# Kernel tuning notes

Measured on AMD Instinct MI355X. Metric: run time of the kernel, lower is better.

The kernel has to match this reference:

```python
import jax, jax.numpy as jnp
import numpy as np

D_MODEL = 1024
NUM_HEAD = 16
D_K = D_MODEL // NUM_HEAD


def setup_inputs() -> dict:
    key = jax.random.key(0)
    ks = jax.random.split(key, 11)
    B, S = 2, 2048
    s = 1.0 / np.sqrt(D_MODEL)
    return {
        "q": jax.random.normal(ks[0], (B, S, D_MODEL), jnp.float32),
        "k": jax.random.normal(ks[1], (B, S, D_MODEL), jnp.float32),
        "v": jax.random.normal(ks[2], (B, S, D_MODEL), jnp.float32),
        "Wq": jax.random.normal(ks[3], (D_MODEL, D_MODEL), jnp.float32) * s,
        "bq": jnp.zeros((D_MODEL,), jnp.float32),
        "Wk": jax.random.normal(ks[4], (D_MODEL, D_MODEL), jnp.float32) * s,
        "bk": jnp.zeros((D_MODEL,), jnp.float32),
        "Wv": jax.random.normal(ks[5], (D_MODEL, D_MODEL), jnp.float32) * s,
        "bv": jnp.zeros((D_MODEL,), jnp.float32),
        "Wo": jax.random.normal(ks[6], (D_MODEL, D_MODEL), jnp.float32) * s,
        "bo": jnp.zeros((D_MODEL,), jnp.float32),
    }


def _split_head(x, B):
    # [B, S, d_model] -> [B, H, S, d_k]
    S = x.shape[1]
    return x.reshape(B, S, NUM_HEAD, D_K).transpose(0, 2, 1, 3)


def reference(q, k, v, Wq, bq, Wk, bk, Wv, bv, Wo, bo):
    B = q.shape[0]
    qh = _split_head(q @ Wq + bq, B)  # [B,H,Sq,dk]
    kh = _split_head(k @ Wk + bk, B)  # [B,H,Sk,dk]
    vh = _split_head(v @ Wv + bv, B)  # [B,H,Sk,dk]
    scores = jnp.einsum("bhqd,bhkd->bhqk", qh, kh) / jnp.sqrt(
        jnp.asarray(D_K, qh.dtype)
    )
    attn = jax.nn.softmax(scores, axis=-1)
    out = jnp.einsum("bhqk,bhkd->bhqd", attn, vh)  # [B,H,Sq,dk]
    out = out.transpose(0, 2, 1, 3).reshape(B, -1, D_MODEL)
    return jax.nn.relu(out @ Wo + bo)
```

## Files before the change

### kernel.cpp

```cpp
#include <hip/hip_runtime.h>
#include <math.h>

#define SEQ 2048
#define NHD 16

typedef float f32x4 __attribute__((ext_vector_type(4), may_alias));
typedef _Float16 h16x8 __attribute__((ext_vector_type(8), may_alias));
typedef _Float16 h16x4 __attribute__((ext_vector_type(4), may_alias));

__device__ __forceinline__ void gl_lds16(const void* g, void* l) {
  __builtin_amdgcn_global_load_lds(
      (const __attribute__((address_space(1))) unsigned int*)g,
      (__attribute__((address_space(3))) unsigned int*)l, 16, 0, 0);
}

struct PrepArgs {
  const float* W[4];
  _Float16* T[4];
  const float* X[3];
  _Float16* H[3];
};

__global__ __launch_bounds__(256) void prep_k(PrepArgs a) {
  __shared__ float tile[64][65];
  const int blk = blockIdx.x;
  const int t = threadIdx.x;
  if (blk < 1024) {
    const int widx = blk >> 8, tl = blk & 255;
    const int nb = (tl & 15) * 64, kb = (tl >> 4) * 64;
    const float* __restrict__ W = a.W[widx];
    _Float16* __restrict__ T = a.T[widx];
    const int c = t & 63, r0 = t >> 6;
#pragma unroll
    for (int i = 0; i < 16; ++i) {
      const int r = i * 4 + r0;
      tile[r][c] = W[(size_t)(kb + r) * 1024 + nb + c];
    }
    __syncthreads();
#pragma unroll
    for (int i = 0; i < 16; ++i) {
      const int n = i * 4 + r0;
      T[(size_t)(nb + n) * 1024 + kb + c] = (_Float16)tile[c][n];
    }
  } else {
    const int b2 = blk - 1024;
    const int z = b2 >> 11, bx = b2 & 2047;
    const float* __restrict__ X = a.X[z];
    _Float16* __restrict__ H = a.H[z];
    const size_t i = ((size_t)bx * 256 + t) * 8;
    const f32x4 f0 = *(const f32x4*)(X + i);
    const f32x4 f1 = *(const f32x4*)(X + i + 4);
    const float fs[8] = {f0.x, f0.y, f0.z, f0.w, f1.x, f1.y, f1.z, f1.w};
    h16x8 o;
#pragma unroll
    for (int j = 0; j < 8; ++j) o[j] = (_Float16)fs[j];
    *(h16x8*)(H + i) = o;
  }
}

__global__ __launch_bounds__(256) void vtrans_k(const unsigned short* __restrict__ Vb,
                                                unsigned short* __restrict__ Vt) {
  __shared__ unsigned short tile[64][65];
  const int t = threadIdx.x;
  const int c = t & 63, r0 = t >> 6;
  const int s0 = blockIdx.x * 64;
  const int bh = blockIdx.y;
#pragma unroll
  for (int i = 0; i < 16; ++i) {
    const int r = i * 4 + r0;
    tile[r][c] = Vb[((size_t)bh * SEQ + s0 + r) * 64 + c];
  }
  __syncthreads();
#pragma unroll
  for (int i = 0; i < 16; ++i) {
    const int d = i * 4 + r0;
    const int sp = ((c & 15) * 4) + (c >> 4);
    Vt[((size_t)bh * 64 + d) * SEQ + s0 + sp] = tile[c][d];
  }
}

struct QKVArgs {
  const _Float16* A[3];
  const _Float16* Bt[3];
  const float* bias[3];
  _Float16* C[3];
};

__global__ __launch_bounds__(256, 4) void gemm_qkv_k(QKVArgs a) {
  __shared__ char smem[16384];
  h16x8* lds8 = (h16x8*)smem;
  const int dblk = blockIdx.x;
  const int z = dblk >> 8;
  const int rb = dblk & 255;
  const int n0 = ((rb >> 3) & 7) * 128;
  const int m0 = ((((rb >> 6) << 3) | (rb & 7))) * 128;
  const _Float16* __restrict__ A = a.A[z];
  const _Float16* __restrict__ Bt = a.Bt[z];
  const float* __restrict__ bias = a.bias[z];
  _Float16* __restrict__ C = a.C[z];

  const int t = threadIdx.x;
  const int l = t & 63, w = t >> 6;
  const int quad = l >> 4, l15 = l & 15;
  const int wm = w >> 1, wn = w & 1;

  const f32x4 z4 = {0.f, 0.f, 0.f, 0.f};
  f32x4 acc[4][4];
#pragma unroll
  for (int i = 0; i < 4; ++i)
#pragma unroll
    for (int j = 0; j < 4; ++j) acc[i][j] = z4;

  for (int k0 = 0; k0 < 1024; k0 += 32) {
#pragma unroll
    for (int it = 0; it < 2; ++it) {
      const int c = it * 4 + w;
      const int rr = c * 16 + l15;
      gl_lds16(A + (size_t)(m0 + rr) * 1024 + k0 + quad * 8, smem + c * 1024);
      gl_lds16(Bt + (size_t)(n0 + rr) * 1024 + k0 + quad * 8, smem + 8192 + c * 1024);
    }
    __syncthreads();
    h16x8 af[4], bf[4];
#pragma unroll
    for (int i = 0; i < 4; ++i) {
      af[i] = lds8[(wm * 4 + i) * 64 + l];
      bf[i] = lds8[512 + (wn * 4 + i) * 64 + l];
    }
#pragma unroll
    for (int i = 0; i < 4; ++i)
#pragma unroll
      for (int j = 0; j < 4; ++j)
        acc[i][j] = __builtin_amdgcn_mfma_f32_16x16x32_f16(af[i], bf[j], acc[i][j], 0, 0, 0);
    __syncthreads();
  }
#pragma unroll
  for (int i = 0; i < 4; ++i)
#pragma unroll
    for (int j = 0; j < 4; ++j) {
      const int col = n0 + wn * 64 + j * 16 + l15;
      const float bv = bias[col];
#pragma unroll
      for (int r = 0; r < 4; ++r) {
        const int row = m0 + wm * 64 + i * 16 + quad * 4 + r;
        const int b = row >> 11, s = row & 2047;
        const int h = col >> 6, d = col & 63;
        C[((size_t)(b * NHD + h) * SEQ + s) * 64 + d] = (_Float16)(acc[i][j][r] + bv);
      }
    }
}

__global__ __launch_bounds__(256, 4) void gemm_o_k(
    const _Float16* __restrict__ Op0, const _Float16* __restrict__ Op1,
    const float* __restrict__ Lp, const _Float16* __restrict__ Bt,
    const float* __restrict__ bias, float* __restrict__ Cf) {
  __shared__ char smem[24576];
  h16x8* lds8 = (h16x8*)smem;
  float* inv_lds = (float*)(smem + 16384);
  const int rb = blockIdx.x;
  const int n0 = ((rb >> 3) & 7) * 128;
  const int m0 = ((((rb >> 6) << 3) | (rb & 7))) * 128;
  const int t = threadIdx.x;
  const int l = t & 63, w = t >> 6;
  const int quad = l >> 4, l15 = l & 15;
  const int wm = w >> 1, wn = w & 1;

#pragma unroll
  for (int e = t; e < 2048; e += 256) {
    const int rl = e >> 4, hh = e & 15;
    const int m = m0 + rl;
    const int b = m >> 11, s = m & 2047;
    const size_t li = (size_t)(b * NHD + hh) * 2048 + s;
    inv_lds[e] = 1.f / (Lp[li] + Lp[65536 + li]);
  }
  __syncthreads();

  const f32x4 z4 = {0.f, 0.f, 0.f, 0.f};
  f32x4 acc[4][4];
#pragma unroll
  for (int i = 0; i < 4; ++i)
#pragma unroll
    for (int j = 0; j < 4; ++j) acc[i][j] = z4;

  for (int k0 = 0; k0 < 1024; k0 += 32) {
#pragma unroll
    for (int it = 0; it < 2; ++it) {
      const int c = it * 4 + w;
      const int rr = c * 16 + l15;
      gl_lds16(Bt + (size_t)(n0 + rr) * 1024 + k0 + quad * 8, smem + 8192 + c * 1024);
    }
    const int head = k0 >> 6;
#pragma unroll
    for (int it = 0; it < 2; ++it) {
      const int row = it * 64 + (t >> 2);
      const int aq = t & 3;
      const int slot = (row >> 4) * 64 + aq * 16 + ((row & 15) ^ (aq * 2));
      const size_t off = (size_t)(m0 + row) * 1024 + k0 + aq * 8;
      const h16x8 a0 = *(const h16x8*)(Op0 + off);
      const h16x8 a1 = *(const h16x8*)(Op1 + off);
      const float inv = inv_lds[row * 16 + head];
      h16x8 hv;
#pragma unroll
      for (int j = 0; j < 8; ++j)
        hv[j] = (_Float16)(((float)a0[j] + (float)a1[j]) * inv);
      lds8[slot] = hv;
    }
    __syncthreads();
    h16x8 af[4], bf[4];
#pragma unroll
    for (int i = 0; i < 4; ++i) {
      af[i] = lds8[(wm * 4 + i) * 64 + quad * 16 + (l15 ^ (quad * 2))];
      bf[i] = lds8[512 + (wn * 4 + i) * 64 + l];
    }
#pragma unroll
    for (int i = 0; i < 4; ++i)
#pragma unroll
      for (int j = 0; j < 4; ++j)
        acc[i][j] = __builtin_amdgcn_mfma_f32_16x16x32_f16(af[i], bf[j], acc[i][j], 0, 0, 0);
    __syncthreads();
  }
#pragma unroll
  for (int i = 0; i < 4; ++i)
#pragma unroll
    for (int j = 0; j < 4; ++j) {
      const int col = n0 + wn * 64 + j * 16 + l15;
      const float bv = bias[col];
#pragma unroll
      for (int r = 0; r < 4; ++r) {
        const int row = m0 + wm * 64 + i * 16 + quad * 4 + r;
        Cf[(size_t)row * 1024 + col] = fmaxf(acc[i][j][r] + bv, 0.f);
      }
    }
}

__global__ __launch_bounds__(256, 4) void attn_k(
    const _Float16* __restrict__ Qf, const _Float16* __restrict__ Kf,
    const _Float16* __restrict__ Vtp,
    _Float16* __restrict__ Op0, _Float16* __restrict__ Op1,
    float* __restrict__ Lp) {
  __shared__ char smem[34816];
  h16x8* lds8 = (h16x8*)smem;
  const int dblk = blockIdx.x;
  const int comb = ((dblk >> 7) << 3) | (dblk & 7);
  const int q0 = ((dblk >> 3) & 15) * 128;
  const int bh = comb >> 1;
  const int kz = comb & 1;
  const int t = threadIdx.x;
  const int l = t & 63, w = t >> 6;
  const int quad = l >> 4, l15 = l & 15;
  const int b = bh >> 4, h = bh & 15;

  const _Float16* Kb = Kf + (size_t)bh * SEQ * 64;
  const _Float16* Vtb = Vtp + (size_t)bh * 64 * SEQ;

  h16x8 qf[2][2];
#pragma unroll
  for (int mi = 0; mi < 2; ++mi) {
    const size_t qb = ((size_t)bh * SEQ + q0 + w * 32 + mi * 16 + l15) * 64;
#pragma unroll
    for (int ks = 0; ks < 2; ++ks)
      qf[mi][ks] = *(const h16x8*)&Qf[qb + ks * 32 + quad * 8];
  }
  const f32x4 z4 = {0.f, 0.f, 0.f, 0.f};
  f32x4 oacc[2][4], lacc[2];
#pragma unroll
  for (int mi = 0; mi < 2; ++mi) {
    lacc[mi] = z4;
#pragma unroll
    for (int i = 0; i < 4; ++i) oacc[mi][i] = z4;
  }
  h16x8 ones;
#pragma unroll
  for (int j = 0; j < 8; ++j) ones[j] = (_Float16)1.0f;

  const int kbeg = kz * 1024;
  for (int k0 = kbeg; k0 < kbeg + 1024; k0 += 64) {
#pragma unroll
    for (int it = 0; it < 2; ++it) {
      const int c = it * 4 + w;
      const int kd = (c >> 1) * 16 + l15;
      const int off2 = (c & 1) * 32 + quad * 8;
      gl_lds16(Kb + (size_t)(k0 + kd) * 64 + off2, smem + c * 1024);
      gl_lds16(Vtb + (size_t)kd * SEQ + k0 + off2, smem + 8192 + c * 1024);
    }
    __syncthreads();

    {
      h16x8 kfr[4][2];
#pragma unroll
      for (int nt = 0; nt < 4; ++nt)
#pragma unroll
        for (int ks = 0; ks < 2; ++ks) kfr[nt][ks] = lds8[(nt * 2 + ks) * 64 + l];

#pragma unroll
      for (int mi = 0; mi < 2; ++mi) {
        f32x4 sacc[4];
#pragma unroll
        for (int nt = 0; nt < 4; ++nt) {
          f32x4 s = z4;
          s = __builtin_amdgcn_mfma_f32_16x16x32_f16(qf[mi][0], kfr[nt][0], s, 0, 0, 0);
          s = __builtin_amdgcn_mfma_f32_16x16x32_f16(qf[mi][1], kfr[nt][1], s, 0, 0, 0);
          sacc[nt] = s;
        }
        char* pb = smem + 16384 + (w * 2 + mi) * 2304;
#pragma unroll
        for (int r = 0; r < 4; ++r) {
          h16x4 pk;
#pragma unroll
          for (int nt = 0; nt < 4; ++nt)
            pk[nt] = (_Float16)__expf(sacc[nt][r] * 0.125f);
          *(h16x4*)(pb + (quad * 4 + r) * 144 + l15 * 8) = pk;
        }
      }
    }
    __asm__ __volatile__("" ::: "memory");

    {
      h16x8 vfr[4][2];
#pragma unroll
      for (int nt = 0; nt < 4; ++nt)
#pragma unroll
        for (int ks = 0; ks < 2; ++ks) vfr[nt][ks] = lds8[512 + (nt * 2 + ks) * 64 + l];

#pragma unroll
      for (int mi = 0; mi < 2; ++mi) {
        char* pb = smem + 16384 + (w * 2 + mi) * 2304;
        const h16x8 pf0 = *(const h16x8*)(pb + l15 * 144 + quad * 16);
        const h16x8 pf1 = *(const h16x8*)(pb + l15 * 144 + 64 + quad * 16);
        lacc[mi] = __builtin_amdgcn_mfma_f32_16x16x32_f16(pf0, ones, lacc[mi], 0, 0, 0);
        lacc[mi] = __builtin_amdgcn_mfma_f32_16x16x32_f16(pf1, ones, lacc[mi], 0, 0, 0);
#pragma unroll
        for (int nt = 0; nt < 4; ++nt) {
          oacc[mi][nt] = __builtin_amdgcn_mfma_f32_16x16x32_f16(pf0, vfr[nt][0], oacc[mi][nt], 0, 0, 0);
          oacc[mi][nt] = __builtin_amdgcn_mfma_f32_16x16x32_f16(pf1, vfr[nt][1], oacc[mi][nt], 0, 0, 0);
        }
      }
    }
    __syncthreads();
  }

  _Float16* __restrict__ Op = kz ? Op1 : Op0;
#pragma unroll
  for (int mi = 0; mi < 2; ++mi)
#pragma unroll
    for (int nt = 0; nt < 4; ++nt)
#pragma unroll
      for (int r = 0; r < 4; ++r) {
        const size_t tok = (size_t)b * SEQ + q0 + w * 32 + mi * 16 + quad * 4 + r;
        Op[tok * 1024 + h * 64 + nt * 16 + l15] = (_Float16)oacc[mi][nt][r];
      }
  if (l15 == 0) {
#pragma unroll
    for (int mi = 0; mi < 2; ++mi)
#pragma unroll
      for (int r = 0; r < 4; ++r) {
        const int row = q0 + w * 32 + mi * 16 + quad * 4 + r;
        Lp[(size_t)kz * 65536 + bh * 2048 + row] = lacc[mi][r];
      }
  }
}

extern "C" void kernel_launch(void* const* d_in, const int* in_sizes, int n_in,
                              void* d_out, int out_size, void* d_ws, size_t ws_size,
                              hipStream_t stream) {
  const float* q = (const float*)d_in[0];
  const float* k = (const float*)d_in[1];
  const float* v = (const float*)d_in[2];
  const float* Wq = (const float*)d_in[3];
  const float* bq = (const float*)d_in[4];
  const float* Wk = (const float*)d_in[5];
  const float* bk = (const float*)d_in[6];
  const float* Wv = (const float*)d_in[7];
  const float* bv = (const float*)d_in[8];
  const float* Wo = (const float*)d_in[9];
  const float* bo = (const float*)d_in[10];

  char* W8 = (char*)d_ws;
  const size_t MB = 1024 * 1024;
  auto F = [&](size_t off) { return (_Float16*)(W8 + off); };
  _Float16* wt[4] = {F(0), F(2 * MB), F(4 * MB), F(6 * MB)};
  _Float16* qf = F(8 * MB);
  _Float16* kf = F(16 * MB);
  _Float16* vf = F(24 * MB);
  _Float16* Qf = F(32 * MB);
  _Float16* Kf = F(40 * MB);
  _Float16* Vb = F(48 * MB);
  _Float16* Vt = F(56 * MB);
  _Float16* Op0 = F(8 * MB);
  _Float16* Op1 = F(16 * MB);
  float* Lp = (float*)(W8 + 64 * MB);

  const dim3 blk(256);

  PrepArgs pa;
  pa.W[0] = Wq; pa.W[1] = Wk; pa.W[2] = Wv; pa.W[3] = Wo;
  pa.T[0] = wt[0]; pa.T[1] = wt[1]; pa.T[2] = wt[2]; pa.T[3] = wt[3];
  pa.X[0] = q; pa.X[1] = k; pa.X[2] = v;
  pa.H[0] = qf; pa.H[1] = kf; pa.H[2] = vf;
  prep_k<<<dim3(7168), blk, 0, stream>>>(pa);

  QKVArgs qa;
  qa.A[0] = qf; qa.A[1] = kf; qa.A[2] = vf;
  qa.Bt[0] = wt[0]; qa.Bt[1] = wt[1]; qa.Bt[2] = wt[2];
  qa.bias[0] = bq; qa.bias[1] = bk; qa.bias[2] = bv;
  qa.C[0] = Qf; qa.C[1] = Kf; qa.C[2] = Vb;
  gemm_qkv_k<<<dim3(768), blk, 0, stream>>>(qa);

  vtrans_k<<<dim3(32, 32), blk, 0, stream>>>((const unsigned short*)Vb,
                                             (unsigned short*)Vt);
  attn_k<<<dim3(1024), blk, 0, stream>>>(Qf, Kf, Vt, Op0, Op1, Lp);
  gemm_o_k<<<dim3(256), blk, 0, stream>>>(Op0, Op1, Lp, wt[3], bo, (float*)d_out);
}
```

Measured before the change: 254.8 us.

## Double-buffer LDS tiles in QKV and output projection GEMMs

Both projection GEMMs now use two LDS buffers. The next K-slice's global-to-LDS loads (and, in the output GEMM, the register prefetch of the attention partials) are issued before the MFMAs on the current slice, and one barrier per iteration replaces two. The aim is to hide global load latency behind matrix math. In exchange, LDS use doubles, which may reduce occupancy, and the output GEMM drops its min-blocks launch bound, which could raise register pressure.

```diff
diff --git a/kernel.cpp b/kernel.cpp
--- a/kernel.cpp
+++ b/kernel.cpp
@@ -87,8 +87,7 @@
 };
 
 __global__ __launch_bounds__(256, 4) void gemm_qkv_k(QKVArgs a) {
-  __shared__ char smem[16384];
-  h16x8* lds8 = (h16x8*)smem;
+  __shared__ char smem[32768];
   const int dblk = blockIdx.x;
   const int z = dblk >> 8;
   const int rb = dblk & 255;
@@ -104,22 +103,31 @@
   const int quad = l >> 4, l15 = l & 15;
   const int wm = w >> 1, wn = w & 1;
 
-  const f32x4 z4 = {0.f, 0.f, 0.f, 0.f};
-  f32x4 acc[4][4];
-#pragma unroll
-  for (int i = 0; i < 4; ++i)
-#pragma unroll
-    for (int j = 0; j < 4; ++j) acc[i][j] = z4;
-
-  for (int k0 = 0; k0 < 1024; k0 += 32) {
+  auto stage = [&](int buf, int k0) {
 #pragma unroll
     for (int it = 0; it < 2; ++it) {
       const int c = it * 4 + w;
       const int rr = c * 16 + l15;
-      gl_lds16(A + (size_t)(m0 + rr) * 1024 + k0 + quad * 8, smem + c * 1024);
-      gl_lds16(Bt + (size_t)(n0 + rr) * 1024 + k0 + quad * 8, smem + 8192 + c * 1024);
-    }
-    __syncthreads();
+      gl_lds16(A + (size_t)(m0 + rr) * 1024 + k0 + quad * 8,
+               smem + buf * 16384 + c * 1024);
+      gl_lds16(Bt + (size_t)(n0 + rr) * 1024 + k0 + quad * 8,
+               smem + buf * 16384 + 8192 + c * 1024);
+    }
+  };
+
+  const f32x4 z4 = {0.f, 0.f, 0.f, 0.f};
+  f32x4 acc[4][4];
+#pragma unroll
+  for (int i = 0; i < 4; ++i)
+#pragma unroll
+    for (int j = 0; j < 4; ++j) acc[i][j] = z4;
+
+  stage(0, 0);
+  __syncthreads();
+  int cur = 0;
+  for (int k0 = 0; k0 < 1024; k0 += 32) {
+    if (k0 + 32 < 1024) stage(cur ^ 1, k0 + 32);
+    const h16x8* lds8 = (const h16x8*)(smem + cur * 16384);
     h16x8 af[4], bf[4];
 #pragma unroll
     for (int i = 0; i < 4; ++i) {
@@ -132,6 +140,7 @@
       for (int j = 0; j < 4; ++j)
         acc[i][j] = __builtin_amdgcn_mfma_f32_16x16x32_f16(af[i], bf[j], acc[i][j], 0, 0, 0);
     __syncthreads();
+    cur ^= 1;
   }
 #pragma unroll
   for (int i = 0; i < 4; ++i)
@@ -149,13 +158,12 @@
     }
 }
 
-__global__ __launch_bounds__(256, 4) void gemm_o_k(
+__global__ __launch_bounds__(256) void gemm_o_k(
     const _Float16* __restrict__ Op0, const _Float16* __restrict__ Op1,
     const float* __restrict__ Lp, const _Float16* __restrict__ Bt,
     const float* __restrict__ bias, float* __restrict__ Cf) {
-  __shared__ char smem[24576];
-  h16x8* lds8 = (h16x8*)smem;
-  float* inv_lds = (float*)(smem + 16384);
+  __shared__ char smem[40960];
+  float* inv_lds = (float*)(smem + 32768);
   const int rb = blockIdx.x;
   const int n0 = ((rb >> 3) & 7) * 128;
   const int m0 = ((((rb >> 6) << 3) | (rb & 7))) * 128;
@@ -163,6 +171,7 @@
   const int l = t & 63, w = t >> 6;
   const int quad = l >> 4, l15 = l & 15;
   const int wm = w >> 1, wn = w & 1;
+  const int arow0 = t >> 2, aq = t & 3;
 
 #pragma unroll
   for (int e = t; e < 2048; e += 256) {
@@ -174,49 +183,74 @@
   }
   __syncthreads();
 
-  const f32x4 z4 = {0.f, 0.f, 0.f, 0.f};
-  f32x4 acc[4][4];
-#pragma unroll
-  for (int i = 0; i < 4; ++i)
-#pragma unroll
-    for (int j = 0; j < 4; ++j) acc[i][j] = z4;
-
-  for (int k0 = 0; k0 < 1024; k0 += 32) {
+  auto stageB = [&](int buf, int k0) {
 #pragma unroll
     for (int it = 0; it < 2; ++it) {
       const int c = it * 4 + w;
       const int rr = c * 16 + l15;
-      gl_lds16(Bt + (size_t)(n0 + rr) * 1024 + k0 + quad * 8, smem + 8192 + c * 1024);
-    }
+      gl_lds16(Bt + (size_t)(n0 + rr) * 1024 + k0 + quad * 8,
+               smem + buf * 8192 + c * 1024);
+    }
+  };
+  auto loadA = [&](int k0, h16x8 (&r0)[2], h16x8 (&r1)[2]) {
+#pragma unroll
+    for (int it = 0; it < 2; ++it) {
+      const size_t off = (size_t)(m0 + it * 64 + arow0) * 1024 + k0 + aq * 8;
+      r0[it] = *(const h16x8*)(Op0 + off);
+      r1[it] = *(const h16x8*)(Op1 + off);
+    }
+  };
+  auto writeA = [&](int buf, int k0, const h16x8 (&r0)[2], const h16x8 (&r1)[2]) {
     const int head = k0 >> 6;
+    h16x8* alds = (h16x8*)(smem + 16384 + buf * 8192);
 #pragma unroll
     for (int it = 0; it < 2; ++it) {
-      const int row = it * 64 + (t >> 2);
-      const int aq = t & 3;
+      const int row = it * 64 + arow0;
       const int slot = (row >> 4) * 64 + aq * 16 + ((row & 15) ^ (aq * 2));
-      const size_t off = (size_t)(m0 + row) * 1024 + k0 + aq * 8;
-      const h16x8 a0 = *(const h16x8*)(Op0 + off);
-      const h16x8 a1 = *(const h16x8*)(Op1 + off);
       const float inv = inv_lds[row * 16 + head];
       h16x8 hv;
 #pragma unroll
       for (int j = 0; j < 8; ++j)
-        hv[j] = (_Float16)(((float)a0[j] + (float)a1[j]) * inv);
-      lds8[slot] = hv;
-    }
-    __syncthreads();
+        hv[j] = (_Float16)(((float)r0[it][j] + (float)r1[it][j]) * inv);
+      alds[slot] = hv;
+    }
+  };
+
+  const f32x4 z4 = {0.f, 0.f, 0.f, 0.f};
+  f32x4 acc[4][4];
+#pragma unroll
+  for (int i = 0; i < 4; ++i)
+#pragma unroll
+    for (int j = 0; j < 4; ++j) acc[i][j] = z4;
+
+  h16x8 a0r[2], a1r[2];
+  loadA(0, a0r, a1r);
+  stageB(0, 0);
+  writeA(0, 0, a0r, a1r);
+  __syncthreads();
+  int cur = 0;
+  for (int k0 = 0; k0 < 1024; k0 += 32) {
+    const int nk = k0 + 32;
+    if (nk < 1024) {
+      loadA(nk, a0r, a1r);
+      stageB(cur ^ 1, nk);
+    }
+    const h16x8* blds = (const h16x8*)(smem + cur * 8192);
+    const h16x8* alds = (const h16x8*)(smem + 16384 + cur * 8192);
     h16x8 af[4], bf[4];
 #pragma unroll
     for (int i = 0; i < 4; ++i) {
-      af[i] = lds8[(wm * 4 + i) * 64 + quad * 16 + (l15 ^ (quad * 2))];
-      bf[i] = lds8[512 + (wn * 4 + i) * 64 + l];
+      af[i] = alds[(wm * 4 + i) * 64 + quad * 16 + (l15 ^ (quad * 2))];
+      bf[i] = blds[(wn * 4 + i) * 64 + l];
     }
 #pragma unroll
     for (int i = 0; i < 4; ++i)
 #pragma unroll
       for (int j = 0; j < 4; ++j)
         acc[i][j] = __builtin_amdgcn_mfma_f32_16x16x32_f16(af[i], bf[j], acc[i][j], 0, 0, 0);
+    if (nk < 1024) writeA(cur ^ 1, nk, a0r, a1r);
     __syncthreads();
+    cur ^= 1;
   }
 #pragma unroll
   for (int i = 0; i < 4; ++i)
```

Measured after the change: 254.4 us. No clear change (-0.2%).
